# Optimization experiments

Measured on AMD Instinct MI355X. Metric: run time of the kernel, lower is better.

Reference implementation:

```python
import jax, jax.numpy as jnp
import numpy as np

B, T = 32, 1024
VOCAB, N_POS = 300, 3001
D, N_HEAD, D_HID, L = 256, 2, 1024, 4
K1_PAD = 4  # kernel 9, padding 4; second conv is kernel 1, padding 0
EPS = 1e-5


def layer_norm(x, g, b):
    m = jnp.mean(x, axis=-1, keepdims=True)
    v = jnp.mean((x - m) ** 2, axis=-1, keepdims=True)
    return (x - m) * jax.lax.rsqrt(v + EPS) * g + b


def setup_inputs() -> dict:
    key = jax.random.key(0)
    ks = jax.random.split(key, 16)
    src_seq = jax.random.randint(ks[0], (B, T), 0, VOCAB)
    src_pos = jnp.broadcast_to(jnp.arange(1, T + 1), (B, T)).astype(jnp.int32)
    word_emb = (0.02 * jax.random.normal(ks[1], (VOCAB, D))).at[0].set(0.0)  # padding_idx=0
    pos_emb = (0.02 * jax.random.normal(ks[2], (N_POS, D))).at[0].set(0.0)
    s = 0.02
    qkv_w = np.sqrt(2.0 / (D + D // N_HEAD)) * jax.random.normal(ks[3], (L, 3 * D, D))
    qkv_b = jnp.zeros((L, 3 * D))
    fc_w = s * jax.random.normal(ks[4], (L, D, D))
    fc_b = jnp.zeros((L, D))
    ln1_g = jnp.ones((L, D)); ln1_b = jnp.zeros((L, D))
    conv1_w = s * jax.random.normal(ks[5], (L, D_HID, D, 9))
    conv1_b = jnp.zeros((L, D_HID))
    conv2_w = s * jax.random.normal(ks[6], (L, D, D_HID, 1))
    conv2_b = jnp.zeros((L, D))
    ln2_g = jnp.ones((L, D)); ln2_b = jnp.zeros((L, D))
    return dict(src_seq=src_seq, src_pos=src_pos, word_emb=word_emb, pos_emb=pos_emb,
                qkv_w=qkv_w, qkv_b=qkv_b, fc_w=fc_w, fc_b=fc_b,
                ln1_g=ln1_g, ln1_b=ln1_b, conv1_w=conv1_w, conv1_b=conv1_b,
                conv2_w=conv2_w, conv2_b=conv2_b, ln2_g=ln2_g, ln2_b=ln2_b)


def encoder(src_seq, src_pos, word_emb, pos_emb, qkv_w, qkv_b, fc_w, fc_b,
            ln1_g, ln1_b, conv1_w, conv1_b, conv2_w, conv2_b, ln2_g, ln2_b):
    non_pad = (src_seq != 0).astype(jnp.float32)[..., None]          # [B,T,1]
    key_pad = (src_seq == 0)[:, None, None, :]                        # [B,1,1,T]
    x = word_emb[src_seq] + pos_emb[src_pos]                          # [B,T,D]
    dk = D // N_HEAD

    def block(x, p):
        qw, qb, fw, fb, g1, be1, w1, b1, w2, b2, g2, be2 = p
        res = x
        h = layer_norm(x, g1, be1)
        qkv = h @ qw.T + qb                                           # [B,T,3D]
        q, k, v = jnp.split(qkv, 3, axis=-1)
        split = lambda t: t.reshape(B, T, N_HEAD, dk).transpose(0, 2, 1, 3)
        q, k, v = split(q), split(k), split(v)
        attn = jnp.einsum('bhqd,bhkd->bhqk', q, k) / jnp.sqrt(jnp.float32(dk))
        attn = jnp.where(key_pad, -jnp.inf, attn)
        attn = jax.nn.softmax(attn, axis=-1)
        o = jnp.einsum('bhqk,bhkd->bhqd', attn, v)
        o = o.transpose(0, 2, 1, 3).reshape(B, T, D)
        x = (o @ fw.T + fb) + res
        x = x * non_pad
        # position-wise conv FFN
        res = x
        h = layer_norm(x, g2, be2).transpose(0, 2, 1)                 # [B,D,T]
        h = jax.lax.conv_general_dilated(h, w1, (1,), [(K1_PAD, K1_PAD)],
                                         dimension_numbers=('NCH', 'OIH', 'NCH'))
        h = jax.nn.relu(h + b1[None, :, None])
        h = jax.lax.conv_general_dilated(h, w2, (1,), [(0, 0)],
                                         dimension_numbers=('NCH', 'OIH', 'NCH'))
        h = h + b2[None, :, None]
        x = h.transpose(0, 2, 1) + res
        x = x * non_pad
        return x, None

    params = (qkv_w, qkv_b, fc_w, fc_b, ln1_g, ln1_b,
              conv1_w, conv1_b, conv2_w, conv2_b, ln2_g, ln2_b)
    x, _ = jax.lax.scan(block, x, params)
    return x, non_pad


def reference(src_seq, src_pos, word_emb, pos_emb, qkv_w, qkv_b, fc_w, fc_b,
              ln1_g, ln1_b, conv1_w, conv1_b, conv2_w, conv2_b, ln2_g, ln2_b):
    return encoder(src_seq, src_pos, word_emb, pos_emb, qkv_w, qkv_b, fc_w, fc_b,
                   ln1_g, ln1_b, conv1_w, conv1_b, conv2_w, conv2_b, ln2_g, ln2_b)
```

## Files before the change

kernel.cpp:

```cpp
#include <hip/hip_runtime.h>


#define B_ 32
#define T_ 1024
#define D_ 256
#define NH_ 2
#define DK_ 128
#define DH_ 1024
#define L_ 4
#define MROWS (B_ * T_)
#define KCONV (D_ * 9)
#define TPAD 1032

typedef unsigned short u16;
typedef short bf16x8 __attribute__((ext_vector_type(8)));
typedef float f32x4 __attribute__((ext_vector_type(4)));
typedef u16 u16x8 __attribute__((ext_vector_type(8)));

__device__ __forceinline__ float bf2f(u16 h) {
    union { unsigned int u; float f; } a;
    a.u = ((unsigned int)h) << 16;
    return a.f;
}

__device__ __forceinline__ u16 f2bf(float f) {
    union { float f; unsigned int u; } a;
    a.f = f;
    unsigned int r = a.u + 0x7fffu + ((a.u >> 16) & 1u);
    return (u16)(r >> 16);
}

__device__ __forceinline__ void glds16(const u16* g, u16* l) {
    __builtin_amdgcn_global_load_lds(
        (const __attribute__((address_space(1))) void*)g,
        (__attribute__((address_space(3))) void*)l, 16, 0, 0);
}

__global__ void detect_kernel(const void* wemb_raw, int* flag) {
    __shared__ int cnt;
    if (threadIdx.x == 0) cnt = 0;
    __syncthreads();
    const u16* p = (const u16*)wemb_raw;
    if (p[256 + threadIdx.x] != 0) atomicAdd(&cnt, 1);
    __syncthreads();
    if (threadIdx.x == 0) *flag = (cnt >= 128) ? 1 : 0;
}

__global__ void cvt_any_kernel(const void* __restrict__ src, u16* __restrict__ dst,
                               int n, const int* __restrict__ flag) {
    int i = blockIdx.x * 256 + threadIdx.x;
    if (i >= n) return;
    if (*flag) dst[i] = ((const u16*)src)[i];
    else       dst[i] = f2bf(((const float*)src)[i]);
}

__global__ void w1_reorder2_kernel(const float* __restrict__ srcf,
                                   const u16* __restrict__ srch,
                                   u16* __restrict__ out, int n,
                                   const int* __restrict__ flag) {
    int idx = blockIdx.x * 256 + threadIdx.x;
    if (idx >= n) return;
    int l  = idx / (DH_ * KCONV);
    int r  = idx % (DH_ * KCONV);
    int oc = r / KCONV;
    int kk = r % KCONV;
    int kpos = kk >> 8;
    int ic   = kk & 255;
    size_t si = (size_t)l * DH_ * D_ * 9 + (oc * D_ + ic) * 9 + kpos;
    out[idx] = (*flag) ? srch[si] : f2bf(srcf[si]);
}

__global__ void sentinel_kernel(void* out, int out_size) {
    int i = blockIdx.x * 256 + threadIdx.x;
    if (i < out_size) ((u16*)out)[i] = 0x42F6;
}


__global__ void embed_kernel(const int* __restrict__ seq, const int* __restrict__ pos,
                             const u16* __restrict__ wemb, const u16* __restrict__ pemb,
                             float* __restrict__ X, float* __restrict__ NP) {
    int row = blockIdx.x;
    int d   = threadIdx.x;
    int s = seq[row];
    int p = pos[row];
    X[(size_t)row * D_ + d] = bf2f(wemb[s * D_ + d]) + bf2f(pemb[p * D_ + d]);
    if (d == 0) NP[row] = (s != 0) ? 1.0f : 0.0f;
}

__global__ void zero_pad_kernel(u16* __restrict__ Hp, int nb) {
    int i = blockIdx.x * 256 + threadIdx.x;
    if (i >= nb * 8 * 256) return;
    int b = i / (8 * 256);
    int r = (i / 256) & 7;
    int d = i & 255;
    int row = (r < 4) ? r : (1024 + r);
    Hp[(size_t)(b * TPAD + row) * D_ + d] = 0;
}

__global__ __launch_bounds__(256)
void ln_kernel(const float* __restrict__ x, const u16* __restrict__ g,
               const u16* __restrict__ bta, u16* __restrict__ outp) {
    int wave = threadIdx.x >> 6, lane = threadIdx.x & 63;
    int row = blockIdx.x * 4 + wave;
    const float* xr = x + (size_t)row * D_;
    float4 v = *(const float4*)&xr[lane * 4];
    float s  = v.x + v.y + v.z + v.w;
    float s2 = v.x * v.x + v.y * v.y + v.z * v.z + v.w * v.w;
#pragma unroll
    for (int d = 1; d < 64; d <<= 1) {
        s  += __shfl_xor(s,  d, 64);
        s2 += __shfl_xor(s2, d, 64);
    }
    float m   = s * (1.0f / 256.0f);
    float var = s2 * (1.0f / 256.0f) - m * m;
    float rr  = rsqrtf(var + 1e-5f);
    size_t orow = (size_t)((row >> 10) * TPAD + 4 + (row & 1023)) * D_;
    float vv[4] = {v.x, v.y, v.z, v.w};
#pragma unroll
    for (int k = 0; k < 4; k++) {
        int d = lane * 4 + k;
        outp[orow + d] = f2bf((vv[k] - m) * rr * bf2f(g[d]) + bf2f(bta[d]));
    }
}

__global__ void out_kernel(const float* __restrict__ X, const float* __restrict__ NP,
                           void* __restrict__ out, int out_size,
                           const int* __restrict__ flag) {
    int i = blockIdx.x * 256 + threadIdx.x;
    if (i >= out_size) return;
    const int n1 = MROWS * D_;
    float v = (i < n1) ? X[i] : NP[i - n1];
    if (*flag) ((u16*)out)[i] = f2bf(v);
    else       ((float*)out)[i] = v;
}

template <int AMAP, int EPI, int K>
__global__ __launch_bounds__(256)
void gemm_mfma(const u16* __restrict__ A, const u16* __restrict__ W,
               const u16* __restrict__ bias, const float* __restrict__ resid,
               const float* __restrict__ mask, void* __restrict__ Cp,
               int M, int N) {
    __shared__ __align__(16) u16 As[128 * 64];
    __shared__ __align__(16) u16 Bs[128 * 64];
    const int tid  = threadIdx.x;
    const int wave = tid >> 6, lane = tid & 63;
    const int quad = lane >> 4, l15 = lane & 15;
    const int m0 = blockIdx.y * 128, n0 = blockIdx.x * 128;
    const int wm = (wave >> 1) * 64, wn = (wave & 1) * 64;
    const int srow = wave * 32;
    const int row8 = lane >> 3;
    const int grp  = ((lane & 7) ^ row8) * 8;
    f32x4 acc[4][4] = {};

    const u16* pa;
    {
        int m = m0 + srow + row8;
        if (AMAP == 0) pa = A + (size_t)m * K + grp;
        else {
            int hr = (m >> 10) * TPAD + (m & 1023) + (AMAP == 1 ? 4 : 0);
            pa = A + (size_t)hr * D_ + grp;
        }
    }
    const u16* pb = W + (size_t)(n0 + srow + row8) * K + grp;
    constexpr size_t rsA = (AMAP == 0) ? (size_t)K : (size_t)D_;
    constexpr size_t rsB = (size_t)K;

    u16* lda = &As[srow * 64];
    u16* ldb = &Bs[srow * 64];
    const int rg = (quad ^ (l15 & 7)) * 8;

    int kpos = 0;
    constexpr int nkt = K / 64;
    for (int t = 0; t < nkt; t++) {
#pragma unroll
        for (int q = 0; q < 4; q++) {
            glds16(pa + (size_t)q * 8 * rsA, lda + q * 8 * 64);
            glds16(pb + (size_t)q * 8 * rsB, ldb + q * 8 * 64);
        }
        if (AMAP == 2) {
            if (kpos == 8) { kpos = 0; pa += 64 - 8 * 256; pb += 64 - 8 * 256; }
            else           { kpos++;  pa += 256;           pb += 256; }
        } else { pa += 64; pb += 64; }
        __builtin_amdgcn_s_waitcnt(0);
        __syncthreads();
#pragma unroll
        for (int ks = 0; ks < 2; ks++) {
            bf16x8 af[4], bfr[4];
#pragma unroll
            for (int i = 0; i < 4; i++)
                af[i] = *(const bf16x8*)&As[(wm + i * 16 + l15) * 64 + (rg ^ (ks * 32))];
#pragma unroll
            for (int j = 0; j < 4; j++)
                bfr[j] = *(const bf16x8*)&Bs[(wn + j * 16 + l15) * 64 + (rg ^ (ks * 32))];
#pragma unroll
            for (int i = 0; i < 4; i++)
#pragma unroll
                for (int j = 0; j < 4; j++)
                    acc[i][j] = __builtin_amdgcn_mfma_f32_16x16x32_bf16(
                        af[i], bfr[j], acc[i][j], 0, 0, 0);
        }
        __syncthreads();
    }

    float bv[4];
#pragma unroll
    for (int j = 0; j < 4; j++) bv[j] = bf2f(bias[n0 + wn + j * 16 + l15]);
#pragma unroll
    for (int i = 0; i < 4; i++) {
#pragma unroll
        for (int r = 0; r < 4; r++) {
            int m = m0 + wm + i * 16 + quad * 4 + r;
            float mk = (EPI == 2) ? mask[m] : 1.0f;
#pragma unroll
            for (int j = 0; j < 4; j++) {
                int n = n0 + wn + j * 16 + l15;
                float v = acc[i][j][r] + bv[j];
                if (EPI == 1) v = fmaxf(v, 0.0f);
                if (EPI == 2) {
                    v = (v + resid[(size_t)m * N + n]) * mk;
                    ((float*)Cp)[(size_t)m * N + n] = v;
                } else {
                    ((u16*)Cp)[(size_t)m * N + n] = f2bf(v);
                }
            }
        }
    }
}

__global__ __launch_bounds__(256, 2)
void attn_mfma(const u16* __restrict__ QKV, const float* __restrict__ NPg,
               u16* __restrict__ Hp) {
    __shared__ __align__(16) u16 KsPs[64 * 136];
    __shared__ __align__(16) u16 Vt[128 * 72];
    __shared__ float npS[1024];
    u16* Ks  = KsPs;
    const int tid  = threadIdx.x;
    const int wave = tid >> 6, lane = tid & 63;
    const int quad = lane >> 4, l15 = lane & 15;
    const int hb = blockIdx.x;
    const int h = hb & (NH_ - 1), b = hb >> 1;
    const int qt8 = blockIdx.y;
    const int t0 = qt8 * 128;
    const float scale = 0.08838834764831845f;
    u16* Psw = KsPs + wave * 16 * 72;

    for (int i = tid; i < 1024; i += 256) npS[i] = NPg[b * 1024 + i];

    bf16x8 q_a[2][4];
#pragma unroll
    for (int sub = 0; sub < 2; sub++)
#pragma unroll
        for (int s = 0; s < 4; s++)
            q_a[sub][s] = *(const bf16x8*)(QKV
                + (size_t)(b * 1024 + t0 + sub * 64 + wave * 16 + l15) * 768
                + h * DK_ + s * 32 + quad * 8);

    float m_st[2][4], l_st[2][4];
    f32x4 oacc[2][8] = {};
#pragma unroll
    for (int sub = 0; sub < 2; sub++)
#pragma unroll
        for (int r = 0; r < 4; r++) { m_st[sub][r] = -1e30f; l_st[sub][r] = 0.0f; }

    u16x8 kpre[4], vpre[4];
    const int skey = tid >> 4;
    const int dk0  = (tid & 15) * 8;
    const int colb0 = ((tid & 7) << 3);
#pragma unroll
    for (int p = 0; p < 4; p++) {
        size_t grow = (size_t)(b * 1024 + 0 + skey + p * 16) * 768 + h * DK_;
        kpre[p] = *(const u16x8*)(QKV + grow + 256 + dk0);
        vpre[p] = *(const u16x8*)(QKV + grow + 512 + dk0);
    }

    for (int kk = 0; kk < 16; kk++) {
        const int k0 = kk * 64;
        if (kk) __syncthreads();
#pragma unroll
        for (int p = 0; p < 4; p++) {
            int key = skey + p * 16;
            *(u16x8*)&Ks[key * 136 + dk0] = kpre[p];
            int colb = key ^ colb0;
#pragma unroll
            for (int e = 0; e < 8; e++) Vt[(dk0 + e) * 72 + colb] = vpre[p][e];
        }
        __syncthreads();
        if (kk < 15) {
#pragma unroll
            for (int p = 0; p < 4; p++) {
                size_t grow = (size_t)(b * 1024 + k0 + 64 + skey + p * 16) * 768 + h * DK_;
                kpre[p] = *(const u16x8*)(QKV + grow + 256 + dk0);
                vpre[p] = *(const u16x8*)(QKV + grow + 512 + dk0);
            }
        }

        f32x4 s4[2][4];
#pragma unroll
        for (int sub = 0; sub < 2; sub++)
#pragma unroll
            for (int nt = 0; nt < 4; nt++) {
                f32x4 c = {0.f, 0.f, 0.f, 0.f};
#pragma unroll
                for (int s = 0; s < 4; s++) {
                    bf16x8 kb = *(const bf16x8*)&Ks[(nt * 16 + l15) * 136 + s * 32 + quad * 8];
                    c = __builtin_amdgcn_mfma_f32_16x16x32_bf16(q_a[sub][s], kb, c, 0, 0, 0);
                }
                s4[sub][nt] = c;
            }
        __syncthreads();

#pragma unroll
        for (int sub = 0; sub < 2; sub++) {
#pragma unroll
            for (int nt = 0; nt < 4; nt++) {
                bool pad = (npS[k0 + nt * 16 + l15] == 0.0f);
#pragma unroll
                for (int r = 0; r < 4; r++)
                    s4[sub][nt][r] = pad ? -1e30f : s4[sub][nt][r] * scale;
            }
            float alpha[4];
#pragma unroll
            for (int r = 0; r < 4; r++) {
                float v = fmaxf(fmaxf(s4[sub][0][r], s4[sub][1][r]),
                                fmaxf(s4[sub][2][r], s4[sub][3][r]));
#pragma unroll
                for (int d = 1; d < 16; d <<= 1) v = fmaxf(v, __shfl_xor(v, d, 64));
                float mnew = fmaxf(m_st[sub][r], v);
                alpha[r] = __expf(m_st[sub][r] - mnew);
                m_st[sub][r] = mnew;
                l_st[sub][r] *= alpha[r];
            }
#pragma unroll
            for (int nt = 0; nt < 4; nt++)
#pragma unroll
                for (int r = 0; r < 4; r++)
                    s4[sub][nt][r] = __expf(s4[sub][nt][r] - m_st[sub][r]);
#pragma unroll
            for (int r = 0; r < 4; r++) {
                float v = s4[sub][0][r] + s4[sub][1][r] + s4[sub][2][r] + s4[sub][3][r];
#pragma unroll
                for (int d = 1; d < 16; d <<= 1) v += __shfl_xor(v, d, 64);
                l_st[sub][r] += v;
            }
#pragma unroll
            for (int dt = 0; dt < 8; dt++)
#pragma unroll
                for (int r = 0; r < 4; r++) oacc[sub][dt][r] *= alpha[r];
#pragma unroll
            for (int nt = 0; nt < 4; nt++)
#pragma unroll
                for (int r = 0; r < 4; r++)
                    Psw[(quad * 4 + r) * 72 + nt * 16 + l15] = f2bf(s4[sub][nt][r]);
#pragma unroll
            for (int ks = 0; ks < 2; ks++) {
                bf16x8 pa = *(const bf16x8*)&Psw[l15 * 72 + ks * 32 + quad * 8];
#pragma unroll
                for (int dt = 0; dt < 8; dt++) {
                    int d = dt * 16 + l15;
                    int swr = ((d >> 3) & 7) << 3;
                    bf16x8 vb = *(const bf16x8*)&Vt[d * 72 + ((ks * 32 + quad * 8) ^ swr)];
                    oacc[sub][dt] = __builtin_amdgcn_mfma_f32_16x16x32_bf16(
                        pa, vb, oacc[sub][dt], 0, 0, 0);
                }
            }
        }
    }

#pragma unroll
    for (int sub = 0; sub < 2; sub++)
#pragma unroll
        for (int r = 0; r < 4; r++) {
            float inv = 1.0f / l_st[sub][r];
            int t = t0 + sub * 64 + wave * 16 + quad * 4 + r;
            size_t orow = (size_t)(b * TPAD + 4 + t) * D_ + h * DK_;
#pragma unroll
            for (int dt = 0; dt < 8; dt++)
                Hp[orow + dt * 16 + l15] = f2bf(oacc[sub][dt][r] * inv);
        }
}


static inline int cdiv(int a, int b) { return (a + b - 1) / b; }

extern "C" void kernel_launch(void* const* d_in, const int* in_sizes, int n_in,
                              void* d_out, int out_size, void* d_ws, size_t ws_size,
                              hipStream_t stream) {
    const int* seq = (const int*)d_in[0];
    const int* pos = (const int*)d_in[1];
    (void)in_sizes; (void)n_in;

    int   cb = 8, w1L = 1;
    int*   FLAG; float* X; float* NP; u16* Hpad; u16* SCR; u16* W1R;
    u16 *WEMB, *PEMB, *QKVW, *QKVB, *FCW, *FCB, *G1c, *B1c, *C1B, *C2W, *C2B, *G2c, *B2c;

    unsigned char* wsb = (unsigned char*)d_ws;
    size_t off;
    auto build = [&](int cb_, int w1L_) -> size_t {
        off = 0;
        auto take = [&](size_t bytes) {
            unsigned char* p = wsb + off;
            off += (bytes + 255) & ~(size_t)255;
            return p;
        };
        FLAG = (int*)  take(4);
        X    = (float*)take((size_t)MROWS * D_ * 4);
        NP   = (float*)take((size_t)MROWS * 4);
        Hpad = (u16*)  take((size_t)cb_ * TPAD * D_ * 2);
        SCR  = (u16*)  take((size_t)cb_ * T_ * DH_ * 2);
        W1R  = (u16*)  take((size_t)w1L_ * DH_ * KCONV * 2);
        WEMB = (u16*)  take((size_t)300 * D_ * 2);
        PEMB = (u16*)  take((size_t)3001 * D_ * 2);
        QKVW = (u16*)  take((size_t)L_ * 3 * D_ * D_ * 2);
        QKVB = (u16*)  take((size_t)L_ * 3 * D_ * 2);
        FCW  = (u16*)  take((size_t)L_ * D_ * D_ * 2);
        FCB  = (u16*)  take((size_t)L_ * D_ * 2);
        G1c  = (u16*)  take((size_t)L_ * D_ * 2);
        B1c  = (u16*)  take((size_t)L_ * D_ * 2);
        C1B  = (u16*)  take((size_t)L_ * DH_ * 2);
        C2W  = (u16*)  take((size_t)L_ * D_ * DH_ * 2);
        C2B  = (u16*)  take((size_t)L_ * D_ * 2);
        G2c  = (u16*)  take((size_t)L_ * D_ * 2);
        B2c  = (u16*)  take((size_t)L_ * D_ * 2);
        return off;
    };
    if      (build(32, L_) <= ws_size) { cb = 32; w1L = L_; }
    else if (build(8,  L_) <= ws_size) { cb = 8;  w1L = L_; }
    else if (build(8,  1)  <= ws_size) { cb = 8;  w1L = 1;  }
    else {
        sentinel_kernel<<<cdiv(out_size, 256), 256, 0, stream>>>(d_out, out_size);
        return;
    }
    const int nch = B_ / cb;
    const int Mc  = cb * T_;

    detect_kernel<<<1, 256, 0, stream>>>(d_in[2], FLAG);
    auto cvt = [&](const void* src, u16* dst, int n) {
        cvt_any_kernel<<<cdiv(n, 256), 256, 0, stream>>>(src, dst, n, FLAG);
    };
    cvt(d_in[2],  WEMB, 300 * D_);
    cvt(d_in[3],  PEMB, 3001 * D_);
    cvt(d_in[4],  QKVW, L_ * 3 * D_ * D_);
    cvt(d_in[5],  QKVB, L_ * 3 * D_);
    cvt(d_in[6],  FCW,  L_ * D_ * D_);
    cvt(d_in[7],  FCB,  L_ * D_);
    cvt(d_in[8],  G1c,  L_ * D_);
    cvt(d_in[9],  B1c,  L_ * D_);
    cvt(d_in[11], C1B,  L_ * DH_);
    cvt(d_in[12], C2W,  L_ * D_ * DH_);
    cvt(d_in[13], C2B,  L_ * D_);
    cvt(d_in[14], G2c,  L_ * D_);
    cvt(d_in[15], B2c,  L_ * D_);
    if (w1L == L_) {
        int n = L_ * DH_ * KCONV;
        w1_reorder2_kernel<<<cdiv(n, 256), 256, 0, stream>>>(
            (const float*)d_in[10], (const u16*)d_in[10], W1R, n, FLAG);
    }

    embed_kernel<<<MROWS, 256, 0, stream>>>(seq, pos, WEMB, PEMB, X, NP);
    zero_pad_kernel<<<cb * 8, 256, 0, stream>>>(Hpad, cb);

    for (int l = 0; l < L_; l++) {
        for (int c = 0; c < nch; c++) {
            const size_t ro = (size_t)c * Mc;
            ln_kernel<<<Mc / 4, 256, 0, stream>>>(
                X + ro * D_, G1c + l * D_, B1c + l * D_, Hpad);
            gemm_mfma<1, 0, 256><<<dim3(6, Mc / 128), 256, 0, stream>>>(
                Hpad, QKVW + (size_t)l * 3 * D_ * D_, QKVB + l * 3 * D_,
                nullptr, nullptr, SCR, Mc, 3 * D_);
            attn_mfma<<<dim3(NH_ * cb, 8), 256, 0, stream>>>(
                SCR, NP + ro, Hpad);
            gemm_mfma<1, 2, 256><<<dim3(2, Mc / 128), 256, 0, stream>>>(
                Hpad, FCW + (size_t)l * D_ * D_, FCB + l * D_,
                X + ro * D_, NP + ro, X + ro * D_, Mc, D_);
        }
        const u16* w1p = W1R + (w1L == L_ ? (size_t)l * DH_ * KCONV : 0);
        if (w1L != L_) {
            int n = DH_ * KCONV;
            w1_reorder2_kernel<<<cdiv(n, 256), 256, 0, stream>>>(
                (const float*)d_in[10] + (size_t)l * DH_ * D_ * 9,
                (const u16*)d_in[10] + (size_t)l * DH_ * D_ * 9,
                W1R, n, FLAG);
        }
        for (int c = 0; c < nch; c++) {
            const size_t ro = (size_t)c * Mc;
            ln_kernel<<<Mc / 4, 256, 0, stream>>>(
                X + ro * D_, G2c + l * D_, B2c + l * D_, Hpad);
            gemm_mfma<2, 1, 2304><<<dim3(8, Mc / 128), 256, 0, stream>>>(
                Hpad, w1p, C1B + l * DH_,
                nullptr, nullptr, SCR, Mc, DH_);
            gemm_mfma<0, 2, 1024><<<dim3(2, Mc / 128), 256, 0, stream>>>(
                SCR, C2W + (size_t)l * D_ * DH_, C2B + l * D_,
                X + ro * D_, NP + ro, X + ro * D_, Mc, D_);
        }
    }

    out_kernel<<<cdiv(out_size, 256), 256, 0, stream>>>(X, NP, d_out, out_size, FLAG);
}
```

Before: 1.688 ms.

## Emit pre-transposed V from QKV GEMM and load attention tiles asynchronously

The QKV GEMM gains an epilogue that writes Q and K into a 512-wide buffer and V in a per-head transposed [d][t] layout. This lets the attention kernel fill its LDS tiles with direct global-to-LDS loads (glds16) using XOR swizzles, instead of register prefetch plus a scalar transpose scatter. The score and PV loops are also restructured so each K/V fragment read from LDS feeds two MFMAs. In exchange, the register prefetch that overlapped the next tile's load with compute is gone: each iteration waits for its own loads to finish. The GEMM epilogue also does extra index math for the transposed V store.

```diff
diff --git a/kernel.cpp b/kernel.cpp
--- a/kernel.cpp
+++ b/kernel.cpp
@@ -139,7 +139,7 @@
 void gemm_mfma(const u16* __restrict__ A, const u16* __restrict__ W,
                const u16* __restrict__ bias, const float* __restrict__ resid,
                const float* __restrict__ mask, void* __restrict__ Cp,
-               int M, int N) {
+               u16* __restrict__ vout, int M, int N) {
     __shared__ __align__(16) u16 As[128 * 64];
     __shared__ __align__(16) u16 Bs[128 * 64];
     const int tid  = threadIdx.x;
@@ -208,41 +208,62 @@
 #pragma unroll
     for (int i = 0; i < 4; i++) {
 #pragma unroll
-        for (int r = 0; r < 4; r++) {
-            int m = m0 + wm + i * 16 + quad * 4 + r;
-            float mk = (EPI == 2) ? mask[m] : 1.0f;
-#pragma unroll
-            for (int j = 0; j < 4; j++) {
-                int n = n0 + wn + j * 16 + l15;
+        for (int j = 0; j < 4; j++) {
+            int n = n0 + wn + j * 16 + l15;
+            int mbase = m0 + wm + i * 16 + quad * 4;
+            float o[4];
+#pragma unroll
+            for (int r = 0; r < 4; r++) {
                 float v = acc[i][j][r] + bv[j];
                 if (EPI == 1) v = fmaxf(v, 0.0f);
-                if (EPI == 2) {
-                    v = (v + resid[(size_t)m * N + n]) * mk;
+                o[r] = v;
+            }
+            if (EPI == 2) {
+#pragma unroll
+                for (int r = 0; r < 4; r++) {
+                    int m = mbase + r;
+                    float v = (o[r] + resid[(size_t)m * N + n]) * mask[m];
                     ((float*)Cp)[(size_t)m * N + n] = v;
+                }
+            } else if (EPI == 3) {
+                if (n0 < 512) {
+#pragma unroll
+                    for (int r = 0; r < 4; r++)
+                        ((u16*)Cp)[(size_t)(mbase + r) * 512 + n] = f2bf(o[r]);
                 } else {
-                    ((u16*)Cp)[(size_t)m * N + n] = f2bf(v);
+                    int dg = n - 512;
+                    int bb = mbase >> 10, tt = mbase & 1023;
+                    ushort4 pk;
+                    pk.x = f2bf(o[0]); pk.y = f2bf(o[1]);
+                    pk.z = f2bf(o[2]); pk.w = f2bf(o[3]);
+                    *(ushort4*)&vout[(size_t)((dg >> 7) + (bb << 1)) * (128 * 1024)
+                                     + (size_t)(dg & 127) * 1024 + tt] = pk;
                 }
+            } else {
+#pragma unroll
+                for (int r = 0; r < 4; r++)
+                    ((u16*)Cp)[(size_t)(mbase + r) * N + n] = f2bf(o[r]);
             }
         }
     }
 }
 
 __global__ __launch_bounds__(256, 2)
-void attn_mfma(const u16* __restrict__ QKV, const float* __restrict__ NPg,
-               u16* __restrict__ Hp) {
-    __shared__ __align__(16) u16 KsPs[64 * 136];
-    __shared__ __align__(16) u16 Vt[128 * 72];
+void attn_mfma(const u16* __restrict__ QKV, const u16* __restrict__ Vg,
+               const float* __restrict__ NPg, u16* __restrict__ Hp) {
+    __shared__ __align__(16) u16 Ks[64 * 128];
+    __shared__ __align__(16) u16 Vt[128 * 64];
+    __shared__ __align__(16) u16 Ps[4 * 32 * 72];
     __shared__ float npS[1024];
-    u16* Ks  = KsPs;
     const int tid  = threadIdx.x;
     const int wave = tid >> 6, lane = tid & 63;
     const int quad = lane >> 4, l15 = lane & 15;
     const int hb = blockIdx.x;
     const int h = hb & (NH_ - 1), b = hb >> 1;
-    const int qt8 = blockIdx.y;
-    const int t0 = qt8 * 128;
+    const int t0 = blockIdx.y * 128;
     const float scale = 0.08838834764831845f;
-    u16* Psw = KsPs + wave * 16 * 72;
+    u16* Psw = Ps + wave * 32 * 72;
+    const u16* Vgh = Vg + (size_t)hb * (128 * 1024);
 
     for (int i = tid; i < 1024; i += 256) npS[i] = NPg[b * 1024 + i];
 
@@ -252,7 +273,7 @@
 #pragma unroll
         for (int s = 0; s < 4; s++)
             q_a[sub][s] = *(const bf16x8*)(QKV
-                + (size_t)(b * 1024 + t0 + sub * 64 + wave * 16 + l15) * 768
+                + (size_t)(b * 1024 + t0 + sub * 64 + wave * 16 + l15) * 512
                 + h * DK_ + s * 32 + quad * 8);
 
     float m_st[2][4], l_st[2][4];
@@ -261,53 +282,36 @@
     for (int sub = 0; sub < 2; sub++)
 #pragma unroll
         for (int r = 0; r < 4; r++) { m_st[sub][r] = -1e30f; l_st[sub][r] = 0.0f; }
-
-    u16x8 kpre[4], vpre[4];
-    const int skey = tid >> 4;
-    const int dk0  = (tid & 15) * 8;
-    const int colb0 = ((tid & 7) << 3);
-#pragma unroll
-    for (int p = 0; p < 4; p++) {
-        size_t grow = (size_t)(b * 1024 + 0 + skey + p * 16) * 768 + h * DK_;
-        kpre[p] = *(const u16x8*)(QKV + grow + 256 + dk0);
-        vpre[p] = *(const u16x8*)(QKV + grow + 512 + dk0);
-    }
 
     for (int kk = 0; kk < 16; kk++) {
         const int k0 = kk * 64;
         if (kk) __syncthreads();
 #pragma unroll
-        for (int p = 0; p < 4; p++) {
-            int key = skey + p * 16;
-            *(u16x8*)&Ks[key * 136 + dk0] = kpre[p];
-            int colb = key ^ colb0;
-#pragma unroll
-            for (int e = 0; e < 8; e++) Vt[(dk0 + e) * 72 + colb] = vpre[p][e];
-        }
+        for (int i = 0; i < 4; i++) {
+            int c = i * 256 + tid;
+            int key = c >> 4, gk = (c & 15) ^ (key & 15);
+            glds16(QKV + (size_t)(b * 1024 + k0 + key) * 512 + 256 + h * DK_ + gk * 8,
+                   Ks + (size_t)(i * 256 + wave * 64) * 8);
+            int d = c >> 3, gv = (c & 7) ^ (d & 7);
+            glds16(Vgh + (size_t)d * 1024 + k0 + gv * 8,
+                   Vt + (size_t)(i * 256 + wave * 64) * 8);
+        }
+        __builtin_amdgcn_s_waitcnt(0);
         __syncthreads();
-        if (kk < 15) {
-#pragma unroll
-            for (int p = 0; p < 4; p++) {
-                size_t grow = (size_t)(b * 1024 + k0 + 64 + skey + p * 16) * 768 + h * DK_;
-                kpre[p] = *(const u16x8*)(QKV + grow + 256 + dk0);
-                vpre[p] = *(const u16x8*)(QKV + grow + 512 + dk0);
-            }
-        }
-
-        f32x4 s4[2][4];
-#pragma unroll
-        for (int sub = 0; sub < 2; sub++)
-#pragma unroll
-            for (int nt = 0; nt < 4; nt++) {
-                f32x4 c = {0.f, 0.f, 0.f, 0.f};
-#pragma unroll
-                for (int s = 0; s < 4; s++) {
-                    bf16x8 kb = *(const bf16x8*)&Ks[(nt * 16 + l15) * 136 + s * 32 + quad * 8];
-                    c = __builtin_amdgcn_mfma_f32_16x16x32_bf16(q_a[sub][s], kb, c, 0, 0, 0);
-                }
-                s4[sub][nt] = c;
-            }
-        __syncthreads();
+
+        f32x4 s4[2][4] = {};
+#pragma unroll
+        for (int nt = 0; nt < 4; nt++) {
+#pragma unroll
+            for (int s = 0; s < 4; s++) {
+                bf16x8 kb = *(const bf16x8*)&Ks[(nt * 16 + l15) * 128
+                                                + ((s * 4 + quad) ^ l15) * 8];
+                s4[0][nt] = __builtin_amdgcn_mfma_f32_16x16x32_bf16(
+                    q_a[0][s], kb, s4[0][nt], 0, 0, 0);
+                s4[1][nt] = __builtin_amdgcn_mfma_f32_16x16x32_bf16(
+                    q_a[1][s], kb, s4[1][nt], 0, 0, 0);
+            }
+        }
 
 #pragma unroll
         for (int sub = 0; sub < 2; sub++) {
@@ -350,18 +354,23 @@
             for (int nt = 0; nt < 4; nt++)
 #pragma unroll
                 for (int r = 0; r < 4; r++)
-                    Psw[(quad * 4 + r) * 72 + nt * 16 + l15] = f2bf(s4[sub][nt][r]);
-#pragma unroll
-            for (int ks = 0; ks < 2; ks++) {
-                bf16x8 pa = *(const bf16x8*)&Psw[l15 * 72 + ks * 32 + quad * 8];
-#pragma unroll
-                for (int dt = 0; dt < 8; dt++) {
-                    int d = dt * 16 + l15;
-                    int swr = ((d >> 3) & 7) << 3;
-                    bf16x8 vb = *(const bf16x8*)&Vt[d * 72 + ((ks * 32 + quad * 8) ^ swr)];
-                    oacc[sub][dt] = __builtin_amdgcn_mfma_f32_16x16x32_bf16(
-                        pa, vb, oacc[sub][dt], 0, 0, 0);
-                }
+                    Psw[(sub * 16 + quad * 4 + r) * 72 + nt * 16 + l15] =
+                        f2bf(s4[sub][nt][r]);
+        }
+
+#pragma unroll
+        for (int ks = 0; ks < 2; ks++) {
+            bf16x8 pa0 = *(const bf16x8*)&Psw[l15 * 72 + ks * 32 + quad * 8];
+            bf16x8 pa1 = *(const bf16x8*)&Psw[(16 + l15) * 72 + ks * 32 + quad * 8];
+#pragma unroll
+            for (int dt = 0; dt < 8; dt++) {
+                int d = dt * 16 + l15;
+                bf16x8 vb = *(const bf16x8*)&Vt[d * 64
+                                                + (((ks * 4 + quad) ^ (d & 7)) * 8)];
+                oacc[0][dt] = __builtin_amdgcn_mfma_f32_16x16x32_bf16(
+                    pa0, vb, oacc[0][dt], 0, 0, 0);
+                oacc[1][dt] = __builtin_amdgcn_mfma_f32_16x16x32_bf16(
+                    pa1, vb, oacc[1][dt], 0, 0, 0);
             }
         }
     }
@@ -462,16 +471,18 @@
     for (int l = 0; l < L_; l++) {
         for (int c = 0; c < nch; c++) {
             const size_t ro = (size_t)c * Mc;
+            u16* QKV = SCR;
+            u16* Vg  = SCR + (size_t)Mc * 512;
             ln_kernel<<<Mc / 4, 256, 0, stream>>>(
                 X + ro * D_, G1c + l * D_, B1c + l * D_, Hpad);
-            gemm_mfma<1, 0, 256><<<dim3(6, Mc / 128), 256, 0, stream>>>(
+            gemm_mfma<1, 3, 256><<<dim3(6, Mc / 128), 256, 0, stream>>>(
                 Hpad, QKVW + (size_t)l * 3 * D_ * D_, QKVB + l * 3 * D_,
-                nullptr, nullptr, SCR, Mc, 3 * D_);
+                nullptr, nullptr, QKV, Vg, Mc, 768);
             attn_mfma<<<dim3(NH_ * cb, 8), 256, 0, stream>>>(
-                SCR, NP + ro, Hpad);
+                QKV, Vg, NP + ro, Hpad);
             gemm_mfma<1, 2, 256><<<dim3(2, Mc / 128), 256, 0, stream>>>(
                 Hpad, FCW + (size_t)l * D_ * D_, FCB + l * D_,
-                X + ro * D_, NP + ro, X + ro * D_, Mc, D_);
+                X + ro * D_, NP + ro, X + ro * D_, nullptr, Mc, D_);
         }
         const u16* w1p = W1R + (w1L == L_ ? (size_t)l * DH_ * KCONV : 0);
         if (w1L != L_) {
@@ -487,10 +498,10 @@
                 X + ro * D_, G2c + l * D_, B2c + l * D_, Hpad);
             gemm_mfma<2, 1, 2304><<<dim3(8, Mc / 128), 256, 0, stream>>>(
                 Hpad, w1p, C1B + l * DH_,
-                nullptr, nullptr, SCR, Mc, DH_);
+                nullptr, nullptr, SCR, nullptr, Mc, DH_);
             gemm_mfma<0, 2, 1024><<<dim3(2, Mc / 128), 256, 0, stream>>>(
                 SCR, C2W + (size_t)l * D_ * DH_, C2B + l * D_,
-                X + ro * D_, NP + ro, X + ro * D_, Mc, D_);
+                X + ro * D_, NP + ro, X + ro * D_, nullptr, Mc, D_);
         }
     }
 
```

Result: faster. 1.543 ms (-8.6%).
